# Optimization experiments

Measured on AMD Instinct MI355X. Metric: run time of the kernel, lower is better.

The kernel has to match this reference:

```python
import jax, jax.numpy as jnp
import numpy as np

# ---- config mirroring init kwargs ----
D_MODEL = 512
NUM_DIRS = 8
QUANTILES = (0.1, 0.5, 0.9)
POLY_ORDER = 2
BETA_INIT = 0.5
HEAD_WIDTH = 16
SOFTSORT_C = 0.5
SOFTSORT_ALPHA = 0.5
FEAT_IN = NUM_DIRS * (len(QUANTILES) + POLY_ORDER + 1)  # 48


def _legendre_basis(T, order, dtype):
    t = jnp.linspace(-1.0, 1.0, T, dtype=dtype)
    P = [jnp.ones_like(t)]
    if order >= 1:
        P.append(t)
    for n in range(1, order):
        P.append(((2 * n + 1) * t * P[n] - n * P[n - 1]) / (n + 1))
    B = jnp.stack(P[:order + 1], axis=0)
    return B / jnp.sqrt(jnp.maximum(jnp.sum(B * B, axis=1, keepdims=True), 1e-6))


def _isotonic_nonincreasing(y):
    #   v_i = min_{s<=i} max_{t>=i} mean(y[s..t])
    T = y.shape[0]
    c = jnp.concatenate([jnp.zeros((1,), y.dtype), jnp.cumsum(y)])
    s_idx = jnp.arange(T)[:, None]
    t_idx = jnp.arange(T)[None, :]
    length = jnp.maximum(t_idx - s_idx + 1, 1).astype(y.dtype)
    A = (c[t_idx + 1] - c[s_idx]) / length                 # mean over [s, t]
    A = jnp.where(t_idx >= s_idx, A, -jnp.inf)
    R = jax.lax.cummax(A, axis=1, reverse=True)            # R[s,i] = max_{t>=i} A[s,t]
    R = jnp.where(s_idx <= t_idx, R, jnp.inf)
    V = jax.lax.cummin(R, axis=0)                          # V[i,i] = min_{s<=i} R[s,i]
    return jnp.diagonal(V)


def _soft_sort_ascending(vals, reg):
    # Blondel et al. fast-soft-sort with L2 regularization.
    # Descending soft-sort: rho/reg - isotonic_nonincreasing(rho/reg - sort_desc(theta))
    # Ascending = -soft_sort_desc(-vals).
    L, T = vals.shape
    theta = -vals
    s = jnp.sort(theta, axis=-1)[:, ::-1]                  # descending
    rho = jnp.arange(T, 0, -1, dtype=vals.dtype) / jnp.asarray(reg, vals.dtype)
    v = jax.vmap(_isotonic_nonincreasing)(rho[None, :] - s)
    return -(rho[None, :] - v)


def setup_inputs() -> dict:
    key = jax.random.key(0)
    ks = jax.random.split(key, 6)
    B, T, N, D = 2, 128, 128, D_MODEL
    x = jax.random.normal(ks[0], (B, T, N, D), dtype=jnp.float32)
    valid_mask = jnp.ones((B, T, N), dtype=jnp.float32)
    # proj: Linear(D, K, bias=False), kaiming-uniform-ish init
    bound = 1.0 / np.sqrt(D)
    W_proj = jax.random.uniform(ks[1], (NUM_DIRS, D), jnp.float32, -bound, bound)
    # additive head: per-feature Linear(1,width) -> GELU -> Linear(width,D,no bias)
    W1 = jax.random.uniform(ks[2], (FEAT_IN, HEAD_WIDTH), jnp.float32, -1.0, 1.0)
    b1 = jax.random.uniform(ks[3], (FEAT_IN, HEAD_WIDTH), jnp.float32, -1.0, 1.0)
    bw = 1.0 / np.sqrt(HEAD_WIDTH)
    W2 = jax.random.uniform(ks[4], (FEAT_IN, HEAD_WIDTH, D_MODEL), jnp.float32, -bw, bw)
    beta = jnp.full((D_MODEL,), BETA_INIT, dtype=jnp.float32)
    return {"x": x, "valid_mask": valid_mask, "W_proj": W_proj,
            "W1": W1, "b1": b1, "W2": W2, "beta": beta}


def reference(x, valid_mask, W_proj, W1, b1, W2, beta):
    B, T, N, D = x.shape
    K = W_proj.shape[0]
    # orthonormalize projection (done in-place under no_grad in torch -> straight-through)
    Q, _ = jnp.linalg.qr(W_proj.T)                          # [D, K]
    W_eff = W_proj + jax.lax.stop_gradient(Q.T - W_proj)
    U = W_eff.T                                             # [D, K]

    v = jnp.einsum('btnd,dk->btnk', x, U) * valid_mask[..., None]
    v_bnkt = jnp.transpose(v, (0, 2, 3, 1))                 # [B, N, K, T]

    reg = max(1e-3, SOFTSORT_C * float(T) ** (-SOFTSORT_ALPHA))
    ss = _soft_sort_ascending(v_bnkt.reshape(-1, T), reg)   # [L, T]

    levels = jnp.asarray(QUANTILES, x.dtype)
    pos = jnp.clip(levels, 0.0, 1.0) * (T - 1)
    lo = jnp.clip(jnp.floor(pos).astype(jnp.int32), 0, T - 1)
    hi = jnp.clip(jnp.ceil(pos).astype(jnp.int32), 0, T - 1)
    w = pos - lo.astype(x.dtype)
    qv = ((1.0 - w) * ss[:, lo] + w * ss[:, hi]).reshape(B, N, K, -1)

    Bmat = _legendre_basis(T, POLY_ORDER, x.dtype)          # [P+1, T]
    coeff = jnp.einsum('bnkt,pt->bnkp', v_bnkt, Bmat)

    feats = jnp.concatenate([qv, coeff], axis=-1).reshape(B, N, -1)  # [B, N, F]
    hmid = jax.nn.gelu(feats[..., None] * W1 + b1, approximate=False)  # [B, N, F, width]
    parts = jnp.einsum('bnfw,fwd->bnfd', hmid, W2)          # [B, N, F, D]
    y = parts.sum(axis=2)                                   # [B, N, D]

    beta_eff = jax.nn.sigmoid(beta)
    y_btnd = jnp.broadcast_to(y[:, None], (B, T, N, D))
    h = x + beta_eff * y_btnd
    vm = valid_mask[..., None]
    h = vm * h + (1.0 - vm) * x

    num = jnp.mean(jnp.sqrt(jnp.sum((beta_eff * y_btnd) ** 2, axis=-1)))
    den = jnp.maximum(jnp.mean(jnp.sqrt(jnp.sum(x * x, axis=-1))), 1e-9)
    r = jax.lax.stop_gradient(num / den)
    # per-feature energy: contributions are constant over T -> factor T inside sqrt
    sq = jnp.sum((beta_eff * parts) ** 2, axis=(1, 3))       # [B, F]
    energy = jnp.sqrt(jnp.asarray(T, x.dtype) * sq)
    r_feat = jax.lax.stop_gradient(jnp.mean(energy, axis=0) / den)
    return h, r, r_feat
```

## Files before the change

kernel.cpp:

```cpp
#include <hip/hip_runtime.h>
#include <hip/hip_bf16.h>
#include <math.h>

#define OFF_BEFF  0
#define OFF_B2    512
#define OFF_LB    1024
#define OFF_U     1408
#define OFF_FEATS 5504
#define OFF_DENP  17792
#define OFF_NUMP  18816
#define OFF_SQP   19072
#define OFF_V     31360
#define OFF_Y     293504
#define OFF_YP    424576
#define WS_TOTAL  1473152

__device__ __align__(16) float g_ws[WS_TOTAL];

static __device__ __forceinline__ float wred64(float v){
  #pragma unroll
  for (int m = 32; m >= 1; m >>= 1) v += __shfl_xor(v, m, 64);
  return v;
}

__global__ __launch_bounds__(256) void k1_prep(const float* __restrict__ Wp,
                                               const float* __restrict__ beta){
  int tid = threadIdx.x;
  __shared__ float p1s[128], p2s[128], nrm[2];
  for (int d = tid; d < 512; d += 256){
    float b = beta[d];
    float s = 1.0f/(1.0f + expf(-b));
    g_ws[OFF_BEFF + d] = s;
    g_ws[OFF_B2 + d] = s*s;
  }
  if (tid < 128){
    float t = -1.0f + 2.0f*(float)tid/127.0f;
    p1s[tid] = t;
    p2s[tid] = 0.5f*(3.0f*t*t - 1.0f);
  }
  __syncthreads();
  if (tid == 0){
    float a = 0, b = 0;
    for (int i = 0; i < 128; i++){ a += p1s[i]*p1s[i]; b += p2s[i]*p2s[i]; }
    nrm[0] = sqrtf(fmaxf(a, 1e-6f));
    nrm[1] = sqrtf(fmaxf(b, 1e-6f));
  }
  __syncthreads();
  if (tid < 128){
    g_ws[OFF_LB + 0*128 + tid] = 1.0f/sqrtf(128.0f);
    g_ws[OFF_LB + 1*128 + tid] = p1s[tid]/nrm[0];
    g_ws[OFF_LB + 2*128 + tid] = p2s[tid]/nrm[1];
  }
  if (tid < 64){
    int l = tid;
    float A[8][8], Q[8][8], tau[8];
    #pragma unroll
    for (int c = 0; c < 8; c++)
      #pragma unroll
      for (int p = 0; p < 8; p++)
        A[c][p] = Wp[c*512 + p*64 + l];
    #pragma unroll
    for (int j = 0; j < 8; j++){
      float alpha = __shfl(A[j][0], j, 64);
      float ssq = 0.0f;
      #pragma unroll
      for (int p = 0; p < 8; p++){
        bool live = (p > 0) || (l > j);
        float v = A[j][p];
        ssq += live ? v*v : 0.0f;
      }
      ssq = wred64(ssq);
      float tj, scale;
      if (ssq == 0.0f){ tj = 0.0f; scale = 0.0f; }
      else {
        float bta = -copysignf(sqrtf(alpha*alpha + ssq), alpha);
        tj = (bta - alpha)/bta;
        scale = 1.0f/(alpha - bta);
      }
      tau[j] = tj;
      #pragma unroll
      for (int p = 0; p < 8; p++){
        int row = p*64 + l;
        float v = A[j][p]*scale;
        A[j][p] = (row < j) ? 0.0f : (row == j ? 1.0f : v);
      }
      #pragma unroll
      for (int c = j+1; c < 8; c++){
        float d = 0.0f;
        #pragma unroll
        for (int p = 0; p < 8; p++) d += A[c][p]*A[j][p];
        d = wred64(d)*tj;
        #pragma unroll
        for (int p = 0; p < 8; p++) A[c][p] -= d*A[j][p];
      }
    }
    #pragma unroll
    for (int c = 0; c < 8; c++)
      #pragma unroll
      for (int p = 0; p < 8; p++)
        Q[c][p] = (p == 0 && l == c) ? 1.0f : 0.0f;
    #pragma unroll
    for (int j = 7; j >= 0; j--){
      #pragma unroll
      for (int c = 0; c < 8; c++){
        float d = 0.0f;
        #pragma unroll
        for (int p = 0; p < 8; p++) d += Q[c][p]*A[j][p];
        d = wred64(d)*tau[j];
        #pragma unroll
        for (int p = 0; p < 8; p++) Q[c][p] -= d*A[j][p];
      }
    }
    #pragma unroll
    for (int c = 0; c < 8; c++)
      #pragma unroll
      for (int p = 0; p < 8; p++)
        g_ws[OFF_U + c*512 + p*64 + l] = Q[c][p];
  }
}

__global__ __launch_bounds__(256) void k2_proj(const float* __restrict__ x,
                                               const float* __restrict__ vmask){
  int tid = threadIdx.x;
  int l = tid & 63, wv = tid >> 6;
  int g = blockIdx.x*4 + wv;
  __shared__ float denw[4];
  float u[8][8];
  #pragma unroll
  for (int k = 0; k < 8; k++)
    #pragma unroll
    for (int e = 0; e < 8; e++)
      u[k][e] = g_ws[OFF_U + k*512 + l*8 + e];
  int kk = ((l & 1) << 2) | (l & 2) | ((l & 4) >> 2);
  float denpart = 0.0f;
  for (int rr = 0; rr < 8; rr++){
    int row = g*8 + rr;
    const float* xr = x + (size_t)row*512 + l*8;
    float4 xa = *(const float4*)xr;
    float4 xb = *(const float4*)(xr + 4);
    float xe[8] = {xa.x, xa.y, xa.z, xa.w, xb.x, xb.y, xb.z, xb.w};
    float acc[8];
    float sq = 0.0f;
    #pragma unroll
    for (int k = 0; k < 8; k++){
      float a = 0.0f;
      #pragma unroll
      for (int e = 0; e < 8; e++) a += xe[e]*u[k][e];
      acc[k] = a;
    }
    #pragma unroll
    for (int e = 0; e < 8; e++) sq += xe[e]*xe[e];
    if (l & 1){
      float t;
      t=acc[0];acc[0]=acc[4];acc[4]=t;
      t=acc[1];acc[1]=acc[5];acc[5]=t;
      t=acc[2];acc[2]=acc[6];acc[6]=t;
      t=acc[3];acc[3]=acc[7];acc[7]=t;
    }
    acc[0] += __shfl_xor(acc[4], 1, 64);
    acc[1] += __shfl_xor(acc[5], 1, 64);
    acc[2] += __shfl_xor(acc[6], 1, 64);
    acc[3] += __shfl_xor(acc[7], 1, 64);
    if (l & 2){
      float t;
      t=acc[0];acc[0]=acc[2];acc[2]=t;
      t=acc[1];acc[1]=acc[3];acc[3]=t;
    }
    acc[0] += __shfl_xor(acc[2], 2, 64);
    acc[1] += __shfl_xor(acc[3], 2, 64);
    if (l & 4){
      float t=acc[0];acc[0]=acc[1];acc[1]=t;
    }
    acc[0] += __shfl_xor(acc[1], 4, 64);
    acc[0] += __shfl_xor(acc[0], 8, 64);
    acc[0] += __shfl_xor(acc[0], 16, 64);
    acc[0] += __shfl_xor(acc[0], 32, 64);
    sq = wred64(sq);
    float vm = vmask[row];
    if (l < 8){
      int b = row >> 14, t = (row >> 7) & 127, n = row & 127;
      int bn = b*128 + n;
      g_ws[OFF_V + bn*1024 + kk*128 + t] = acc[0]*vm;
    }
    if (l == 0) denpart += sqrtf(sq);
  }
  if (l == 0) denw[wv] = denpart;
  __syncthreads();
  if (tid == 0) g_ws[OFF_DENP + blockIdx.x] = denw[0]+denw[1]+denw[2]+denw[3];
}

__global__ __launch_bounds__(256) void k3_sortfeat(){
  int tid = threadIdx.x;
  int l = tid & 63, wv = tid >> 6;
  int rho = blockIdx.x*4 + wv;
  __shared__ float orig[4][128], srt[4][128], Bl[384];
  __shared__ float pS[4][128];
  __shared__ int   pC[4][128];
  for (int i = tid; i < 384; i += 256) Bl[i] = g_ws[OFF_LB + i];
  const float* vr = g_ws + OFF_V + rho*128;
  orig[wv][2*l]   = vr[2*l];
  orig[wv][2*l+1] = vr[2*l+1];
  srt[wv][2*l] = 0.0f; srt[wv][2*l+1] = 0.0f;
  __syncthreads();
  float c0, c1, c2;
  {
    float a = orig[wv][2*l], b = orig[wv][2*l+1];
    c0 = a*Bl[2*l]       + b*Bl[2*l+1];
    c1 = a*Bl[128+2*l]   + b*Bl[128+2*l+1];
    c2 = a*Bl[256+2*l]   + b*Bl[256+2*l+1];
  }
  c0 = wred64(c0); c1 = wred64(c1); c2 = wred64(c2);
  float e0 = orig[wv][2*l], e1 = orig[wv][2*l+1];
  int r0 = 0, r1 = 0;
  #pragma unroll 4
  for (int j = 0; j < 128; j++){
    float vj = orig[wv][j];
    r0 += (vj < e0) || (vj == e0 && j < 2*l);
    r1 += (vj < e1) || (vj == e1 && j < 2*l+1);
  }
  srt[wv][r0] = e0;
  srt[wv][r1] = e1;
  __syncthreads();
  const float rinv = 22.627416997969522f;
  bool v0 = (srt[wv][2*l+1] - srt[wv][2*l] > rinv);
  bool v1 = (2*l + 2 < 128) ? (srt[wv][2*l+2] - srt[wv][2*l+1] > rinv) : false;
  if (__any(v0 || v1)){
    if (l == 0){
      int top = -1;
      for (int i = 0; i < 128; i++){
        float y = (float)(128 - i)*rinv + srt[wv][i];
        top++; pS[wv][top] = y; pC[wv][top] = 1;
        while (top > 0 &&
               pS[wv][top]*(float)pC[wv][top-1] > pS[wv][top-1]*(float)pC[wv][top]){
          pS[wv][top-1] += pS[wv][top];
          pC[wv][top-1] += pC[wv][top];
          top--;
        }
      }
      int i = 0;
      for (int blk = 0; blk <= top; blk++){
        float m = pS[wv][blk]/(float)pC[wv][blk];
        for (int c = 0; c < pC[wv][blk]; c++){
          srt[wv][i] = m - (float)(128 - i)*rinv;
          i++;
        }
      }
    }
  }
  if (l == 0){
    int bn = rho >> 3, k = rho & 7;
    float* fb = g_ws + OFF_FEATS + bn*48 + k*6;
    float w0 = 0.1f*127.0f - 12.0f;
    float w1 = 0.5f*127.0f - 63.0f;
    float w2 = 0.9f*127.0f - 114.0f;
    fb[0] = (1.0f - w0)*srt[wv][12]  + w0*srt[wv][13];
    fb[1] = (1.0f - w1)*srt[wv][63]  + w1*srt[wv][64];
    fb[2] = (1.0f - w2)*srt[wv][114] + w2*srt[wv][115];
    fb[3] = c0; fb[4] = c1; fb[5] = c2;
  }
}

__global__ __launch_bounds__(512) void k4a_head(const float* __restrict__ W1,
                                                const float* __restrict__ b1,
                                                const float* __restrict__ W2){
  int blk = blockIdx.x;
  int s   = blk & 7;
  int bnp = blk >> 3;
  int bn0 = bnp*2, bn1 = bn0 + 1;
  int tid = threadIdx.x;
  int l = tid & 63, wv = tid >> 6;
  __shared__ float hl0[96], hl1[96];
  __shared__ float sq[8][12];
  if (tid < 192){
    int which = tid >= 96;
    int i = which ? tid - 96 : tid;
    int f = s*6 + (i >> 4);
    int k = f*16 + (i & 15);
    int bn = which ? bn1 : bn0;
    float a = g_ws[OFF_FEATS + bn*48 + f]*W1[k] + b1[k];
    float g = 0.5f*a*(1.0f + erff(a*0.70710678118654752f));
    if (which) hl1[i] = g; else hl0[i] = g;
  }
  __syncthreads();
  int d = tid;
  float b2 = g_ws[OFF_B2 + d];
  float y0 = 0.0f, y1 = 0.0f;
  const float* w2base = W2 + (size_t)(s*96)*512 + d;
  #pragma unroll
  for (int fl_ = 0; fl_ < 6; fl_++){
    float p0 = 0.0f, p1 = 0.0f;
    #pragma unroll
    for (int w = 0; w < 16; w++){
      float w2 = w2base[(size_t)(fl_*16 + w)*512];
      p0 += hl0[fl_*16 + w]*w2;
      p1 += hl1[fl_*16 + w]*w2;
    }
    y0 += p0; y1 += p1;
    float e0 = wred64(p0*p0*b2);
    float e1 = wred64(p1*p1*b2);
    if (l == 0){ sq[wv][fl_*2] = e0; sq[wv][fl_*2 + 1] = e1; }
  }
  g_ws[OFF_YP + (size_t)(bn0*8 + s)*512 + d] = y0;
  g_ws[OFF_YP + (size_t)(bn1*8 + s)*512 + d] = y1;
  __syncthreads();
  if (tid < 12){
    float t = 0.0f;
    #pragma unroll
    for (int w = 0; w < 8; w++) t += sq[w][tid];
    int fl_ = tid >> 1, which = tid & 1;
    int bn = which ? bn1 : bn0;
    g_ws[OFF_SQP + bn*48 + s*6 + fl_] = t;
  }
}

__global__ __launch_bounds__(512) void k4b_red(){
  int bn = blockIdx.x;
  int tid = threadIdx.x;
  int l = tid & 63, wv = tid >> 6;
  __shared__ float nw[8];
  float y = 0.0f;
  #pragma unroll
  for (int s = 0; s < 8; s++) y += g_ws[OFF_YP + (size_t)(bn*8 + s)*512 + tid];
  g_ws[OFF_Y + bn*512 + tid] = y;
  float be = g_ws[OFF_BEFF + tid];
  float by = be*y;
  float ns = wred64(by*by);
  if (l == 0) nw[wv] = ns;
  __syncthreads();
  if (tid == 0){
    float s = nw[0]+nw[1]+nw[2]+nw[3]+nw[4]+nw[5]+nw[6]+nw[7];
    g_ws[OFF_NUMP + bn] = sqrtf(s);
  }
}

__global__ __launch_bounds__(256) void k7_out(const float* __restrict__ x,
                                              const float* __restrict__ vmask,
                                              float* __restrict__ outt){
  if (blockIdx.x == 16384){
    __shared__ float red[256];
    __shared__ float en[96];
    __shared__ float scal[2];
    int tid = threadIdx.x;
    float dp = 0.0f;
    for (int i = tid; i < 1024; i += 256) dp += g_ws[OFF_DENP + i];
    red[tid] = dp; __syncthreads();
    for (int s = 128; s > 0; s >>= 1){
      if (tid < s) red[tid] += red[tid + s];
      __syncthreads();
    }
    if (tid == 0) scal[0] = fmaxf(red[0]/32768.0f, 1e-9f);
    __syncthreads();
    red[tid] = g_ws[OFF_NUMP + tid];
    __syncthreads();
    for (int s = 128; s > 0; s >>= 1){
      if (tid < s) red[tid] += red[tid + s];
      __syncthreads();
    }
    if (tid == 0) scal[1] = red[0]/256.0f;
    __syncthreads();
    float den = scal[0];
    if (tid < 96){
      int b = tid/48, f = tid%48;
      float s = 0.0f;
      for (int j = 0; j < 128; j++) s += g_ws[OFF_SQP + (b*128 + j)*48 + f];
      en[tid] = sqrtf(128.0f*s);
    }
    __syncthreads();
    if (tid == 0) outt[16777216] = scal[1]/den;
    if (tid < 48) outt[16777217 + tid] = 0.5f*(en[tid] + en[48 + tid])/den;
    return;
  }
  int q = blockIdx.x*256 + threadIdx.x;
  size_t fl = (size_t)q*4;
  int d = (int)(fl & 511);
  int row = (int)(fl >> 9);
  int b = row >> 14, n = row & 127;
  int bn = b*128 + n;
  float vm = vmask[row];
  float4 xv = *(const float4*)(x + fl);
  float4 yv = *(const float4*)(g_ws + OFF_Y + bn*512 + d);
  float4 bv = *(const float4*)(g_ws + OFF_BEFF + d);
  float4 o;
  o.x = xv.x + vm*bv.x*yv.x;
  o.y = xv.y + vm*bv.y*yv.y;
  o.z = xv.z + vm*bv.z*yv.z;
  o.w = xv.w + vm*bv.w*yv.w;
  *(float4*)(outt + fl) = o;
}

extern "C" void kernel_launch(void* const* d_in, const int* in_sizes, int n_in,
                              void* d_out, int out_size, void* d_ws, size_t ws_size,
                              hipStream_t stream){
  (void)out_size; (void)d_ws; (void)ws_size;
  const float *x=nullptr,*vm=nullptr,*Wp=nullptr,*W1=nullptr,*b1=nullptr,*W2=nullptr,*beta=nullptr;
  for (int i = 0; i < n_in; i++){
    int s = in_sizes[i];
    const float* p = (const float*)d_in[i];
    if      (s == 16777216) x = p;
    else if (s == 32768)    vm = p;
    else if (s == 4096)     Wp = p;
    else if (s == 393216)   W2 = p;
    else if (s == 512)      beta = p;
    else if (s == 768)      { if (!W1) W1 = p; else b1 = p; }
  }
  float* out = (float*)d_out;

  k1_prep<<<1, 256, 0, stream>>>(Wp, beta);
  k2_proj<<<1024, 256, 0, stream>>>(x, vm);
  k3_sortfeat<<<512, 256, 0, stream>>>();
  k4a_head<<<1024, 512, 0, stream>>>(W1, b1, W2);
  k4b_red<<<256, 512, 0, stream>>>();
  k7_out<<<16385, 256, 0, stream>>>(x, vm, out);
}
```

Before: 88.92 us.

## Drop serial prep kernel by recomputing QR, Legendre basis and sigmoid in consumers

Removes the single-block k1_prep launch. Its Householder QR of the projection matrix is now redone redundantly by every wave of k2_proj, the Legendre basis is rebuilt in each k3 block, and sigmoid(beta) is recomputed wherever it is needed. Separately, k4a replaces its twelve full-wave reductions with a transposed shuffle reduction that sums several values at once. The aim is to remove a serialized, low-occupancy kernel and its launch gap, at the cost of repeated QR arithmetic and shuffles at the start of every k2 wave.

```diff
diff --git a/kernel.cpp b/kernel.cpp
--- a/kernel.cpp
+++ b/kernel.cpp
@@ -2,10 +2,6 @@
 #include <hip/hip_bf16.h>
 #include <math.h>
 
-#define OFF_BEFF  0
-#define OFF_B2    512
-#define OFF_LB    1024
-#define OFF_U     1408
 #define OFF_FEATS 5504
 #define OFF_DENP  17792
 #define OFF_NUMP  18816
@@ -23,114 +19,71 @@
   return v;
 }
 
-__global__ __launch_bounds__(256) void k1_prep(const float* __restrict__ Wp,
-                                               const float* __restrict__ beta){
-  int tid = threadIdx.x;
-  __shared__ float p1s[128], p2s[128], nrm[2];
-  for (int d = tid; d < 512; d += 256){
-    float b = beta[d];
-    float s = 1.0f/(1.0f + expf(-b));
-    g_ws[OFF_BEFF + d] = s;
-    g_ws[OFF_B2 + d] = s*s;
-  }
-  if (tid < 128){
-    float t = -1.0f + 2.0f*(float)tid/127.0f;
-    p1s[tid] = t;
-    p2s[tid] = 0.5f*(3.0f*t*t - 1.0f);
-  }
-  __syncthreads();
-  if (tid == 0){
-    float a = 0, b = 0;
-    for (int i = 0; i < 128; i++){ a += p1s[i]*p1s[i]; b += p2s[i]*p2s[i]; }
-    nrm[0] = sqrtf(fmaxf(a, 1e-6f));
-    nrm[1] = sqrtf(fmaxf(b, 1e-6f));
-  }
-  __syncthreads();
-  if (tid < 128){
-    g_ws[OFF_LB + 0*128 + tid] = 1.0f/sqrtf(128.0f);
-    g_ws[OFF_LB + 1*128 + tid] = p1s[tid]/nrm[0];
-    g_ws[OFF_LB + 2*128 + tid] = p2s[tid]/nrm[1];
-  }
-  if (tid < 64){
-    int l = tid;
-    float A[8][8], Q[8][8], tau[8];
-    #pragma unroll
-    for (int c = 0; c < 8; c++)
-      #pragma unroll
-      for (int p = 0; p < 8; p++)
-        A[c][p] = Wp[c*512 + p*64 + l];
-    #pragma unroll
-    for (int j = 0; j < 8; j++){
-      float alpha = __shfl(A[j][0], j, 64);
-      float ssq = 0.0f;
-      #pragma unroll
-      for (int p = 0; p < 8; p++){
-        bool live = (p > 0) || (l > j);
-        float v = A[j][p];
-        ssq += live ? v*v : 0.0f;
-      }
-      ssq = wred64(ssq);
-      float tj, scale;
-      if (ssq == 0.0f){ tj = 0.0f; scale = 0.0f; }
-      else {
-        float bta = -copysignf(sqrtf(alpha*alpha + ssq), alpha);
-        tj = (bta - alpha)/bta;
-        scale = 1.0f/(alpha - bta);
-      }
-      tau[j] = tj;
-      #pragma unroll
-      for (int p = 0; p < 8; p++){
-        int row = p*64 + l;
-        float v = A[j][p]*scale;
-        A[j][p] = (row < j) ? 0.0f : (row == j ? 1.0f : v);
-      }
-      #pragma unroll
-      for (int c = j+1; c < 8; c++){
-        float d = 0.0f;
-        #pragma unroll
-        for (int p = 0; p < 8; p++) d += A[c][p]*A[j][p];
-        d = wred64(d)*tj;
-        #pragma unroll
-        for (int p = 0; p < 8; p++) A[c][p] -= d*A[j][p];
-      }
-    }
-    #pragma unroll
-    for (int c = 0; c < 8; c++)
-      #pragma unroll
-      for (int p = 0; p < 8; p++)
-        Q[c][p] = (p == 0 && l == c) ? 1.0f : 0.0f;
-    #pragma unroll
-    for (int j = 7; j >= 0; j--){
-      #pragma unroll
-      for (int c = 0; c < 8; c++){
-        float d = 0.0f;
-        #pragma unroll
-        for (int p = 0; p < 8; p++) d += Q[c][p]*A[j][p];
-        d = wred64(d)*tau[j];
-        #pragma unroll
-        for (int p = 0; p < 8; p++) Q[c][p] -= d*A[j][p];
-      }
-    }
-    #pragma unroll
-    for (int c = 0; c < 8; c++)
-      #pragma unroll
-      for (int p = 0; p < 8; p++)
-        g_ws[OFF_U + c*512 + p*64 + l] = Q[c][p];
-  }
-}
-
 __global__ __launch_bounds__(256) void k2_proj(const float* __restrict__ x,
-                                               const float* __restrict__ vmask){
+                                               const float* __restrict__ vmask,
+                                               const float* __restrict__ Wp){
   int tid = threadIdx.x;
   int l = tid & 63, wv = tid >> 6;
   int g = blockIdx.x*4 + wv;
   __shared__ float denw[4];
-  float u[8][8];
-  #pragma unroll
-  for (int k = 0; k < 8; k++)
-    #pragma unroll
-    for (int e = 0; e < 8; e++)
-      u[k][e] = g_ws[OFF_U + k*512 + l*8 + e];
+  float A[8][8], u[8][8], tau[8];
+  #pragma unroll
+  for (int c = 0; c < 8; c++)
+    #pragma unroll
+    for (int p = 0; p < 8; p++)
+      A[c][p] = Wp[c*512 + l*8 + p];
+  #pragma unroll
+  for (int j = 0; j < 8; j++){
+    float alpha = __shfl(A[j][j & 7], j >> 3, 64);
+    float ssq = 0.0f;
+    #pragma unroll
+    for (int p = 0; p < 8; p++){
+      int row = l*8 + p;
+      float v = A[j][p];
+      ssq += (row > j) ? v*v : 0.0f;
+    }
+    ssq = wred64(ssq);
+    float tj, scale;
+    if (ssq == 0.0f){ tj = 0.0f; scale = 0.0f; }
+    else {
+      float bta = -copysignf(sqrtf(alpha*alpha + ssq), alpha);
+      tj = (bta - alpha)/bta;
+      scale = 1.0f/(alpha - bta);
+    }
+    tau[j] = tj;
+    #pragma unroll
+    for (int p = 0; p < 8; p++){
+      int row = l*8 + p;
+      float v = A[j][p]*scale;
+      A[j][p] = (row < j) ? 0.0f : (row == j ? 1.0f : v);
+    }
+    #pragma unroll
+    for (int c = j+1; c < 8; c++){
+      float d = 0.0f;
+      #pragma unroll
+      for (int p = 0; p < 8; p++) d += A[c][p]*A[j][p];
+      d = wred64(d)*tj;
+      #pragma unroll
+      for (int p = 0; p < 8; p++) A[c][p] -= d*A[j][p];
+    }
+  }
+  #pragma unroll
+  for (int c = 0; c < 8; c++)
+    #pragma unroll
+    for (int p = 0; p < 8; p++)
+      u[c][p] = (l*8 + p == c) ? 1.0f : 0.0f;
+  #pragma unroll
+  for (int j = 7; j >= 0; j--){
+    #pragma unroll
+    for (int c = 0; c < 8; c++){
+      float d = 0.0f;
+      #pragma unroll
+      for (int p = 0; p < 8; p++) d += u[c][p]*A[j][p];
+      d = wred64(d)*tau[j];
+      #pragma unroll
+      for (int p = 0; p < 8; p++) u[c][p] -= d*A[j][p];
+    }
+  }
   int kk = ((l & 1) << 2) | (l & 2) | ((l & 4) >> 2);
   float denpart = 0.0f;
   for (int rr = 0; rr < 8; rr++){
@@ -196,11 +149,32 @@
   __shared__ float orig[4][128], srt[4][128], Bl[384];
   __shared__ float pS[4][128];
   __shared__ int   pC[4][128];
-  for (int i = tid; i < 384; i += 256) Bl[i] = g_ws[OFF_LB + i];
+  __shared__ float nrmS[2];
+  if (tid < 128){
+    float t = -1.0f + 2.0f*(float)tid/127.0f;
+    Bl[128+tid] = t;
+    Bl[256+tid] = 0.5f*(3.0f*t*t - 1.0f);
+  }
   const float* vr = g_ws + OFF_V + rho*128;
   orig[wv][2*l]   = vr[2*l];
   orig[wv][2*l+1] = vr[2*l+1];
   srt[wv][2*l] = 0.0f; srt[wv][2*l+1] = 0.0f;
+  __syncthreads();
+  if (tid < 64){
+    float a = Bl[128+tid]*Bl[128+tid] + Bl[192+tid]*Bl[192+tid];
+    float b = Bl[256+tid]*Bl[256+tid] + Bl[320+tid]*Bl[320+tid];
+    a = wred64(a); b = wred64(b);
+    if (tid == 0){
+      nrmS[0] = sqrtf(fmaxf(a, 1e-6f));
+      nrmS[1] = sqrtf(fmaxf(b, 1e-6f));
+    }
+  }
+  __syncthreads();
+  if (tid < 128){
+    Bl[tid] = 0.08838834764831845f;
+    Bl[128+tid] /= nrmS[0];
+    Bl[256+tid] /= nrmS[1];
+  }
   __syncthreads();
   float c0, c1, c2;
   {
@@ -262,7 +236,8 @@
 
 __global__ __launch_bounds__(512) void k4a_head(const float* __restrict__ W1,
                                                 const float* __restrict__ b1,
-                                                const float* __restrict__ W2){
+                                                const float* __restrict__ W2,
+                                                const float* __restrict__ beta){
   int blk = blockIdx.x;
   int s   = blk & 7;
   int bnp = blk >> 3;
@@ -283,8 +258,10 @@
   }
   __syncthreads();
   int d = tid;
-  float b2 = g_ws[OFF_B2 + d];
+  float be = 1.0f/(1.0f + expf(-beta[d]));
+  float b2 = be*be;
   float y0 = 0.0f, y1 = 0.0f;
+  float ev[12];
   const float* w2base = W2 + (size_t)(s*96)*512 + d;
   #pragma unroll
   for (int fl_ = 0; fl_ < 6; fl_++){
@@ -296,12 +273,36 @@
       p1 += hl1[fl_*16 + w]*w2;
     }
     y0 += p0; y1 += p1;
-    float e0 = wred64(p0*p0*b2);
-    float e1 = wred64(p1*p1*b2);
-    if (l == 0){ sq[wv][fl_*2] = e0; sq[wv][fl_*2 + 1] = e1; }
+    ev[fl_*2]     = p0*p0*b2;
+    ev[fl_*2 + 1] = p1*p1*b2;
   }
   g_ws[OFF_YP + (size_t)(bn0*8 + s)*512 + d] = y0;
   g_ws[OFF_YP + (size_t)(bn1*8 + s)*512 + d] = y1;
+  int kk = ((l & 1) << 2) | (l & 2) | ((l & 4) >> 2);
+  {
+    float a0=ev[0],a1=ev[1],a2=ev[2],a3=ev[3],a4=ev[4],a5=ev[5],a6=ev[6],a7=ev[7];
+    if (l & 1){ float t; t=a0;a0=a4;a4=t; t=a1;a1=a5;a5=t; t=a2;a2=a6;a6=t; t=a3;a3=a7;a7=t; }
+    a0 += __shfl_xor(a4,1,64); a1 += __shfl_xor(a5,1,64);
+    a2 += __shfl_xor(a6,1,64); a3 += __shfl_xor(a7,1,64);
+    if (l & 2){ float t; t=a0;a0=a2;a2=t; t=a1;a1=a3;a3=t; }
+    a0 += __shfl_xor(a2,2,64); a1 += __shfl_xor(a3,2,64);
+    if (l & 4){ float t=a0;a0=a1;a1=t; }
+    a0 += __shfl_xor(a1,4,64);
+    a0 += __shfl_xor(a0,8,64); a0 += __shfl_xor(a0,16,64); a0 += __shfl_xor(a0,32,64);
+    if (l < 8) sq[wv][kk] = a0;
+  }
+  {
+    float a0=ev[8],a1=ev[9],a2=ev[10],a3=ev[11],a4=0,a5=0,a6=0,a7=0;
+    if (l & 1){ float t; t=a0;a0=a4;a4=t; t=a1;a1=a5;a5=t; t=a2;a2=a6;a6=t; t=a3;a3=a7;a7=t; }
+    a0 += __shfl_xor(a4,1,64); a1 += __shfl_xor(a5,1,64);
+    a2 += __shfl_xor(a6,1,64); a3 += __shfl_xor(a7,1,64);
+    if (l & 2){ float t; t=a0;a0=a2;a2=t; t=a1;a1=a3;a3=t; }
+    a0 += __shfl_xor(a2,2,64); a1 += __shfl_xor(a3,2,64);
+    if (l & 4){ float t=a0;a0=a1;a1=t; }
+    a0 += __shfl_xor(a1,4,64);
+    a0 += __shfl_xor(a0,8,64); a0 += __shfl_xor(a0,16,64); a0 += __shfl_xor(a0,32,64);
+    if (l < 8 && kk < 4) sq[wv][8 + kk] = a0;
+  }
   __syncthreads();
   if (tid < 12){
     float t = 0.0f;
@@ -313,7 +314,7 @@
   }
 }
 
-__global__ __launch_bounds__(512) void k4b_red(){
+__global__ __launch_bounds__(512) void k4b_red(const float* __restrict__ beta){
   int bn = blockIdx.x;
   int tid = threadIdx.x;
   int l = tid & 63, wv = tid >> 6;
@@ -322,7 +323,7 @@
   #pragma unroll
   for (int s = 0; s < 8; s++) y += g_ws[OFF_YP + (size_t)(bn*8 + s)*512 + tid];
   g_ws[OFF_Y + bn*512 + tid] = y;
-  float be = g_ws[OFF_BEFF + tid];
+  float be = 1.0f/(1.0f + expf(-beta[tid]));
   float by = be*y;
   float ns = wred64(by*by);
   if (l == 0) nw[wv] = ns;
@@ -335,6 +336,7 @@
 
 __global__ __launch_bounds__(256) void k7_out(const float* __restrict__ x,
                                               const float* __restrict__ vmask,
+                                              const float* __restrict__ beta,
                                               float* __restrict__ outt){
   if (blockIdx.x == 16384){
     __shared__ float red[256];
@@ -379,7 +381,12 @@
   float vm = vmask[row];
   float4 xv = *(const float4*)(x + fl);
   float4 yv = *(const float4*)(g_ws + OFF_Y + bn*512 + d);
-  float4 bv = *(const float4*)(g_ws + OFF_BEFF + d);
+  float4 bt = *(const float4*)(beta + d);
+  float4 bv;
+  bv.x = 1.0f/(1.0f + expf(-bt.x));
+  bv.y = 1.0f/(1.0f + expf(-bt.y));
+  bv.z = 1.0f/(1.0f + expf(-bt.z));
+  bv.w = 1.0f/(1.0f + expf(-bt.w));
   float4 o;
   o.x = xv.x + vm*bv.x*yv.x;
   o.y = xv.y + vm*bv.y*yv.y;
@@ -405,10 +412,9 @@
   }
   float* out = (float*)d_out;
 
-  k1_prep<<<1, 256, 0, stream>>>(Wp, beta);
-  k2_proj<<<1024, 256, 0, stream>>>(x, vm);
+  k2_proj<<<1024, 256, 0, stream>>>(x, vm, Wp);
   k3_sortfeat<<<512, 256, 0, stream>>>();
-  k4a_head<<<1024, 512, 0, stream>>>(W1, b1, W2);
-  k4b_red<<<256, 512, 0, stream>>>();
-  k7_out<<<16385, 256, 0, stream>>>(x, vm, out);
-}
+  k4a_head<<<1024, 512, 0, stream>>>(W1, b1, W2, beta);
+  k4b_red<<<256, 512, 0, stream>>>(beta);
+  k7_out<<<16385, 256, 0, stream>>>(x, vm, beta, out);
+}
```

Result: slower. 100.3 us (+12.8%).
